# Optimization experiments

Hardware: AMD Instinct MI355X
Metric: run time of the kernel (lower is better)

The kernel has to match this reference:

```python
import jax, jax.numpy as jnp
import numpy as np

B = 8
A = 1614
TOPN = 6
IOU_THR = 0.25
PAD = 224
OUT = 224

def _make_anchors():
    # 6 anchor shapes on the 14x14 map, 6 on 7x7, 9 on 4x4 -> 1614 total,
    # ordered anchor-type-major then row-major spatial to match the [C,H,W] flatten
    # of the tidy conv outputs (as generate_default_anchor_maps does in NTS-Net).
    specs = [
        (14, 32.0, [(48, 48), (64, 48), (48, 64), (80, 80), (96, 64), (64, 96)]),
        (7, 64.0, [(96, 96), (128, 96), (96, 128), (160, 160), (192, 128), (128, 192)]),
        (4, 112.0, [(192, 192), (256, 192), (192, 256), (288, 288), (320, 256), (256, 320), (352, 352), (384, 320), (320, 384)]),
    ]
    blocks = []
    for fm, stride, sizes in specs:
        c = (np.arange(fm) + 0.5) * stride
        cy, cx = np.meshgrid(c, c, indexing='ij')
        for (h, w) in sizes:
            blocks.append(np.stack([cy - h / 2, cx - w / 2, cy + h / 2, cx + w / 2], -1).reshape(-1, 4))
    a = (np.concatenate(blocks, 0) + PAD).astype(np.int64)  # mimic (edge_anchors+224).astype(int)
    return a.astype(np.float32)  # [1614,4] (y0,x0,y1,x1) in padded-image coords

def _conv(x, w, b, stride, pad):
    y = jax.lax.conv_general_dilated(x, w, (stride, stride), [(pad, pad), (pad, pad)],
                                     dimension_numbers=('NCHW', 'OIHW', 'NCHW'))
    return y + b[None, :, None, None]

def _rpn_scores(rpn, wd1, bd1, wd2, bd2, wd3, bd3, wt1, bt1, wt2, bt2, wt3, bt3):
    b = rpn.shape[0]
    d1 = jax.nn.relu(_conv(rpn, wd1, bd1, 1, 1))   # [B,128,14,14]
    d2 = jax.nn.relu(_conv(d1, wd2, bd2, 2, 1))    # [B,128,7,7]
    d3 = jax.nn.relu(_conv(d2, wd3, bd3, 2, 1))    # [B,128,4,4]
    t1 = _conv(d1, wt1, bt1, 1, 0).reshape(b, -1)  # [B,1176]
    t2 = _conv(d2, wt2, bt2, 1, 0).reshape(b, -1)  # [B,294]
    t3 = _conv(d3, wt3, bt3, 1, 0).reshape(b, -1)  # [B,144]
    return jnp.concatenate([t1, t2, t3], axis=1)   # [B,1614]

def _nms_keep(boxes, scores):
    # Greedy NMS over all A anchors; returns keep mask in ORIGINAL anchor order.
    order = jnp.argsort(-scores)
    b = boxes[order]
    y0, x0, y1, x1 = b[:, 0], b[:, 1], b[:, 2], b[:, 3]
    area = (y1 - y0) * (x1 - x0)
    ih = jnp.clip(jnp.minimum(y1[:, None], y1[None, :]) - jnp.maximum(y0[:, None], y0[None, :]), 0)
    iw = jnp.clip(jnp.minimum(x1[:, None], x1[None, :]) - jnp.maximum(x0[:, None], x0[None, :]), 0)
    inter = ih * iw
    iou = inter / (area[:, None] + area[None, :] - inter)
    idx = jnp.arange(A)
    def body(i, supp):
        row = (iou[i] > IOU_THR) & (idx > i)
        return jnp.where(supp[i], supp, supp | row)
    supp = jax.lax.fori_loop(0, A, body, jnp.zeros((A,), bool))
    return jnp.zeros((A,), bool).at[order].set(~supp)

def _crop_resize(img, box):
    # img [3,Hp,Wp]; box int32 (x0,y0,x1,y1).
    # Equivalent to F.interpolate(img[:, y0:y1, x0:x1], (224,224), 'bilinear', align_corners=True)
    x0, y0, x1, y1 = box[0], box[1], box[2], box[3]
    t = jnp.arange(OUT, dtype=jnp.float32) / (OUT - 1)
    sy = y0.astype(jnp.float32) + t * (y1 - 1 - y0).astype(jnp.float32)
    sx = x0.astype(jnp.float32) + t * (x1 - 1 - x0).astype(jnp.float32)
    y0i = jnp.floor(sy).astype(jnp.int32); x0i = jnp.floor(sx).astype(jnp.int32)
    y1i = jnp.minimum(y0i + 1, y1 - 1);    x1i = jnp.minimum(x0i + 1, x1 - 1)
    wy = (sy - y0i.astype(jnp.float32))[None, :, None]
    wx = (sx - x0i.astype(jnp.float32))[None, None, :]
    g = lambda yi, xi: img[:, yi][:, :, xi]  # gather rows then cols -> [3,224,224]
    top = (1 - wx) * g(y0i, x0i) + wx * g(y0i, x1i)
    bot = (1 - wx) * g(y1i, x0i) + wx * g(y1i, x1i)
    return (1 - wy) * top + wy * bot

def setup_inputs():
    key = jax.random.key(0)
    ks = jax.random.split(key, 16)
    n = jax.random.normal
    return {
        'x': n(ks[0], (B, 3, 448, 448), jnp.float32),
        'rpn_feature': n(ks[1], (B, 2048, 14, 14), jnp.float32),
        'anchors': jnp.asarray(_make_anchors()),
        'wd1': 0.02 * n(ks[2], (128, 2048, 3, 3), jnp.float32), 'bd1': 0.01 * n(ks[3], (128,), jnp.float32),
        'wd2': 0.05 * n(ks[4], (128, 128, 3, 3), jnp.float32),  'bd2': 0.01 * n(ks[5], (128,), jnp.float32),
        'wd3': 0.05 * n(ks[6], (128, 128, 3, 3), jnp.float32),  'bd3': 0.01 * n(ks[7], (128,), jnp.float32),
        'wt1': 0.1 * n(ks[8], (6, 128, 1, 1), jnp.float32),     'bt1': 0.01 * n(ks[9], (6,), jnp.float32),
        'wt2': 0.1 * n(ks[10], (6, 128, 1, 1), jnp.float32),    'bt2': 0.01 * n(ks[11], (6,), jnp.float32),
        'wt3': 0.1 * n(ks[12], (9, 128, 1, 1), jnp.float32),    'bt3': 0.01 * n(ks[13], (9,), jnp.float32),
    }

def reference(x, rpn_feature, anchors, wd1, bd1, wd2, bd2, wd3, bd3, wt1, bt1, wt2, bt2, wt3, bt3):
    scores = _rpn_scores(rpn_feature, wd1, bd1, wd2, bd2, wd3, bd3, wt1, bt1, wt2, bt2, wt3, bt3)
    keep = jax.vmap(lambda s: _nms_keep(anchors, s))(scores)           # [B,A] bool
    masked = jnp.where(keep, scores, -jnp.inf)
    top_prob, top_idx = jax.lax.top_k(masked, TOPN)                    # [B,6]
    tb = anchors[top_idx]                                              # [B,6,4] (y0,x0,y1,x1)
    coords = jnp.stack([tb[..., 1], tb[..., 0], tb[..., 3], tb[..., 2]], -1)  # (x0,y0,x1,y1)
    x_pad = jnp.pad(x, ((0, 0), (0, 0), (PAD, PAD), (PAD, PAD)))       # [B,3,896,896]
    bint = coords.astype(jnp.int32)
    part_imgs = jax.vmap(lambda img, bs: jax.vmap(lambda bb: _crop_resize(img, bb))(bs))(x_pad, bint)  # [B,6,3,224,224]
    return part_imgs, coords, top_prob, top_idx
```

## Files before the change

kernel.cpp:

```cpp
#include <hip/hip_runtime.h>
#include <hip/hip_bf16.h>
#include <math.h>
#include <stdint.h>


#define OFF_COORDS 7225344
#define OFF_PROB   7225536
#define OFF_IDX    7225584
#define NA 1614
#define K1TOT 18432

typedef __attribute__((ext_vector_type(8)))  short  short8;
typedef __attribute__((ext_vector_type(16))) float  floatx16;

__device__ inline void split_bf16(float v, unsigned short& h, unsigned short& l)
{
    __hip_bfloat16 hb = __float2bfloat16(v);
    float hv = __bfloat162float(hb);
    __hip_bfloat16 lb = __float2bfloat16(v - hv);
    h = *reinterpret_cast<unsigned short*>(&hb);
    l = *reinterpret_cast<unsigned short*>(&lb);
}

__global__ __launch_bounds__(256) void k_prep_a(const float* __restrict__ rpn,
                                                __hip_bfloat16* __restrict__ ah,
                                                __hip_bfloat16* __restrict__ al)
{
    __shared__ float tile[64][65];
    const int cib  = blockIdx.x * 64;
    const int posb = blockIdx.y * 64;
    const int b    = blockIdx.z;
    const int t    = threadIdx.x;
#pragma unroll
    for (int it = 0; it < 16; ++it) {
        int idx  = it * 256 + t;
        int cil  = idx >> 6;
        int posl = idx & 63;
        int pos  = posb + posl;
        int py = pos >> 4, px = pos & 15;
        int y = py - 1, x = px - 1;
        float v = 0.0f;
        if ((unsigned)y < 14u && (unsigned)x < 14u)
            v = rpn[((size_t)(b * 2048 + cib + cil) * 14 + y) * 14 + x];
        tile[cil][posl] = v;
    }
    __syncthreads();
#pragma unroll
    for (int it = 0; it < 16; ++it) {
        int idx  = it * 256 + t;
        int posl = idx >> 6;
        int cil  = idx & 63;
        float v = tile[cil][posl];
        unsigned short h, l;
        split_bf16(v, h, l);
        size_t o = (size_t)(b * 256 + posb + posl) * 2048 + cib + cil;
        ((unsigned short*)ah)[o] = h;
        ((unsigned short*)al)[o] = l;
    }
}

__global__ __launch_bounds__(256) void k_prep_b(const float* __restrict__ w,
                                                __hip_bfloat16* __restrict__ bh,
                                                __hip_bfloat16* __restrict__ bl)
{
    __shared__ float tile[9][260];
    const int ci0 = blockIdx.x * 256;
    const int co  = blockIdx.y;
    const int t   = threadIdx.x;
    const float* wc = w + (size_t)co * K1TOT + (size_t)ci0 * 9;
#pragma unroll
    for (int it = 0; it < 9; ++it) {
        int i = it * 256 + t;
        float v = wc[i];
        tile[i % 9][i / 9] = v;
    }
    __syncthreads();
#pragma unroll
    for (int tap = 0; tap < 9; ++tap) {
        float v = tile[tap][t];
        unsigned short h, l;
        split_bf16(v, h, l);
        size_t o = (size_t)co * K1TOT + (size_t)tap * 2048 + ci0 + t;
        ((unsigned short*)bh)[o] = h;
        ((unsigned short*)bl)[o] = l;
    }
}

__global__ __launch_bounds__(128) void k_prep_w23(const float* __restrict__ w2,
                                                  const float* __restrict__ w3,
                                                  __hip_bfloat16* __restrict__ b2h,
                                                  __hip_bfloat16* __restrict__ b2l,
                                                  __hip_bfloat16* __restrict__ b3h,
                                                  __hip_bfloat16* __restrict__ b3l)
{
    const int tap = blockIdx.x;
    const int co  = blockIdx.y;
    const int z   = blockIdx.z;
    const int ci  = threadIdx.x;
    const float* w = z ? w3 : w2;
    __hip_bfloat16* bh = z ? b3h : b2h;
    __hip_bfloat16* bl = z ? b3l : b2l;
    float v = w[((size_t)co * 128 + ci) * 9 + tap];
    unsigned short h, l;
    split_bf16(v, h, l);
    size_t o = (size_t)co * 1152 + tap * 128 + ci;
    ((unsigned short*)bh)[o] = h;
    ((unsigned short*)bl)[o] = l;
}

template<int POSN, int OW, int STR, int CIN, int MTOT, int GX>
__global__ __launch_bounds__(256) void k_conv_mfma(const short* __restrict__ ah,
                                                   const short* __restrict__ al,
                                                   const short* __restrict__ bh,
                                                   const short* __restrict__ bl,
                                                   float* __restrict__ partial,
                                                   int chunk)
{
    constexpr int KTOT = CIN * 9;
    __shared__ short AsH[128][40];
    __shared__ short AsL[128][40];
    __shared__ short BsH[128][40];
    __shared__ short BsL[128][40];

    const int t     = threadIdx.x;
    const int lane  = t & 63;
    const int w     = t >> 6;
    const int wm    = (w & 1) * 64;
    const int wn    = (w >> 1) * 64;
    const int lm    = lane & 31;
    const int half  = lane >> 5;

    const int nb = gridDim.x;
    const int id = blockIdx.x;
    int mb, kc;
    if ((nb % (8 * GX)) == 0) {
        int xcd = id & 7;
        int j   = id >> 3;
        int jq  = j / GX;
        mb = j - jq * GX;
        kc = xcd + 8 * jq;
    } else {
        kc = id / GX;
        mb = id - kc * GX;
    }
    const int mbase = mb * 128;
    const int k0    = kc * chunk;
    const int k1    = (k0 + chunk < KTOT) ? (k0 + chunk) : KTOT;

    int arow[2], apos[2]; bool aval[2];
    const int akc = (t & 3) * 8;
#pragma unroll
    for (int i = 0; i < 2; ++i) {
        int row = ((i * 256 + t) >> 2);
        int m   = mbase + row;
        arow[i] = row;
        aval[i] = (m < MTOT);
        int mm = aval[i] ? m : 0;
        int b  = mm / POSN;
        int p  = mm - b * POSN;
        int y  = p / OW;
        int x  = p - y * OW;
        apos[i] = b * 256 + y * STR * 16 + x * STR;
    }

    floatx16 acc[2][2];
#pragma unroll
    for (int mf = 0; mf < 2; ++mf)
#pragma unroll
        for (int nf = 0; nf < 2; ++nf)
#pragma unroll
            for (int r = 0; r < 16; ++r) acc[mf][nf][r] = 0.0f;

    const short8 zero8 = {0, 0, 0, 0, 0, 0, 0, 0};
    short8 rAh[2], rAl[2], rBh[2], rBl[2];

    auto stage_load = [&](int ks) {
        const int tap = ks / CIN;
        const int ci0 = ks - tap * CIN;
        const int dy  = tap / 3, dx = tap - dy * 3;
#pragma unroll
        for (int i = 0; i < 2; ++i) {
            if (aval[i]) {
                size_t g = (size_t)(apos[i] + dy * 16 + dx) * CIN + ci0 + akc;
                rAh[i] = *(const short8*)(ah + g);
                rAl[i] = *(const short8*)(al + g);
            } else { rAh[i] = zero8; rAl[i] = zero8; }
        }
#pragma unroll
        for (int i = 0; i < 2; ++i) {
            int n = ((i * 256 + t) >> 2);
            size_t g = (size_t)n * KTOT + ks + akc;
            rBh[i] = *(const short8*)(bh + g);
            rBl[i] = *(const short8*)(bl + g);
        }
    };

    if (k0 < k1) stage_load(k0);

    for (int ks = k0; ks < k1; ks += 32) {
#pragma unroll
        for (int i = 0; i < 2; ++i) {
            *(short8*)&AsH[arow[i]][akc] = rAh[i];
            *(short8*)&AsL[arow[i]][akc] = rAl[i];
        }
#pragma unroll
        for (int i = 0; i < 2; ++i) {
            int n = ((i * 256 + t) >> 2);
            *(short8*)&BsH[n][akc] = rBh[i];
            *(short8*)&BsL[n][akc] = rBl[i];
        }
        __syncthreads();
        if (ks + 32 < k1) stage_load(ks + 32);
#pragma unroll
        for (int kst = 0; kst < 2; ++kst) {
            const int koff = kst * 16 + half * 8;
            short8 a_h[2], a_l[2], b_h[2], b_l[2];
#pragma unroll
            for (int mf = 0; mf < 2; ++mf) {
                a_h[mf] = *(const short8*)&AsH[wm + mf * 32 + lm][koff];
                a_l[mf] = *(const short8*)&AsL[wm + mf * 32 + lm][koff];
            }
#pragma unroll
            for (int nf = 0; nf < 2; ++nf) {
                b_h[nf] = *(const short8*)&BsH[wn + nf * 32 + lm][koff];
                b_l[nf] = *(const short8*)&BsL[wn + nf * 32 + lm][koff];
            }
#pragma unroll
            for (int mf = 0; mf < 2; ++mf)
#pragma unroll
                for (int nf = 0; nf < 2; ++nf) {
                    acc[mf][nf] = __builtin_amdgcn_mfma_f32_32x32x16_bf16(
                        a_h[mf], b_h[nf], acc[mf][nf], 0, 0, 0);
                    acc[mf][nf] = __builtin_amdgcn_mfma_f32_32x32x16_bf16(
                        a_h[mf], b_l[nf], acc[mf][nf], 0, 0, 0);
                    acc[mf][nf] = __builtin_amdgcn_mfma_f32_32x32x16_bf16(
                        a_l[mf], b_h[nf], acc[mf][nf], 0, 0, 0);
                }
        }
        __syncthreads();
    }

    float* P = partial + (size_t)kc * MTOT * 128;
#pragma unroll
    for (int mf = 0; mf < 2; ++mf)
#pragma unroll
        for (int nf = 0; nf < 2; ++nf)
#pragma unroll
            for (int r = 0; r < 16; ++r) {
                int row = (r & 3) + 8 * (r >> 2) + 4 * half;
                int m = mbase + wm + mf * 32 + row;
                int n = wn + nf * 32 + lm;
                if (m < MTOT) P[(size_t)m * 128 + n] = acc[mf][nf][r];
            }
}

template<int POSN, int OWV>
__global__ __launch_bounds__(256) void k_reduce_pad(const float* __restrict__ partial,
                                                    const float* __restrict__ bias,
                                                    float* __restrict__ dn,
                                                    __hip_bfloat16* __restrict__ ph,
                                                    __hip_bfloat16* __restrict__ pl,
                                                    int S)
{
    constexpr int MTOT = 8 * POSN;
    int idx = blockIdx.x * 256 + threadIdx.x;
    int b   = idx >> 13;
    int pos = (idx >> 5) & 255;
    int c4  = idx & 31;
    int y = (pos >> 4) - 1;
    int x = (pos & 15) - 1;
    if ((unsigned)y < (unsigned)OWV && (unsigned)x < (unsigned)OWV) {
        int m = b * POSN + y * OWV + x;
        float4 s = ((const float4*)bias)[c4];
        for (int k = 0; k < S; ++k) {
            float4 p = ((const float4*)(partial + (size_t)k * MTOT * 128 + (size_t)m * 128))[c4];
            s.x += p.x; s.y += p.y; s.z += p.z; s.w += p.w;
        }
        s.x = fmaxf(s.x, 0.0f); s.y = fmaxf(s.y, 0.0f);
        s.z = fmaxf(s.z, 0.0f); s.w = fmaxf(s.w, 0.0f);
        ((float4*)dn)[(size_t)m * 32 + c4] = s;
        ushort4 h, l;
        split_bf16(s.x, h.x, l.x);
        split_bf16(s.y, h.y, l.y);
        split_bf16(s.z, h.z, l.z);
        split_bf16(s.w, h.w, l.w);
        ((ushort4*)ph)[idx] = h;
        ((ushort4*)pl)[idx] = l;
    } else {
        ushort4 z = {0, 0, 0, 0};
        ((ushort4*)ph)[idx] = z;
        ((ushort4*)pl)[idx] = z;
    }
}

__global__ __launch_bounds__(256) void k_reduce3(const float* __restrict__ partial,
                                                 const float* __restrict__ bias,
                                                 float* __restrict__ dn, int S)
{
    int idx = blockIdx.x * 256 + threadIdx.x;
    int c4  = idx & 31;
    float4 s = ((const float4*)bias)[c4];
    for (int k = 0; k < S; ++k) {
        float4 p = ((const float4*)(partial + (size_t)k * 128 * 128))[idx];
        s.x += p.x; s.y += p.y; s.z += p.z; s.w += p.w;
    }
    s.x = fmaxf(s.x, 0.0f); s.y = fmaxf(s.y, 0.0f);
    s.z = fmaxf(s.z, 0.0f); s.w = fmaxf(s.w, 0.0f);
    ((float4*)dn)[idx] = s;
}

__global__ __launch_bounds__(256) void k_heads(const float* __restrict__ d1n,
                                               const float* __restrict__ d2n,
                                               const float* __restrict__ d3n,
                                               const float* __restrict__ w1, const float* __restrict__ b1,
                                               const float* __restrict__ w2, const float* __restrict__ b2,
                                               const float* __restrict__ w3, const float* __restrict__ b3,
                                               float* __restrict__ scores)
{
    int idx = blockIdx.x * 256 + threadIdx.x;
    if (idx >= 8 * NA) return;
    int b = idx / NA;
    int e = idx - b * NA;
    const float* d; const float* w; float bias;
    if (e < 1176) {
        int c = e / 196, p = e - c * 196;
        d = d1n + (size_t)(b * 196 + p) * 128; w = w1 + c * 128; bias = b1[c];
    } else if (e < 1470) {
        int e2 = e - 1176; int c = e2 / 49, p = e2 - c * 49;
        d = d2n + (size_t)(b * 49 + p) * 128; w = w2 + c * 128; bias = b2[c];
    } else {
        int e2 = e - 1470; int c = e2 / 16, p = e2 - c * 16;
        d = d3n + (size_t)(b * 16 + p) * 128; w = w3 + c * 128; bias = b3[c];
    }
    float s = bias;
#pragma unroll
    for (int i = 0; i < 32; ++i) {
        float4 dv = ((const float4*)d)[i];
        float4 wv = ((const float4*)w)[i];
        s = fmaf(dv.x, wv.x, s);
        s = fmaf(dv.y, wv.y, s);
        s = fmaf(dv.z, wv.z, s);
        s = fmaf(dv.w, wv.w, s);
    }
    scores[idx] = s;
}

__global__ __launch_bounds__(256) void k_nms_topk(const float* __restrict__ scores,
                                                  const float* __restrict__ anchors,
                                                  float* __restrict__ out,
                                                  int* __restrict__ boxes)
{
    __shared__ float ms[NA];
    __shared__ float ay0[NA], ax0[NA], ay1[NA], ax1[NA];
    __shared__ unsigned char picked[NA];
    __shared__ float rv[4]; __shared__ int ri[4];
    __shared__ float win[5];
    int b = blockIdx.x;
    int t = threadIdx.x;
    for (int i = t; i < NA; i += 256) {
        ms[i] = scores[b * NA + i];
        float4 an = ((const float4*)anchors)[i];
        ay0[i] = an.x; ax0[i] = an.y; ay1[i] = an.z; ax1[i] = an.w;
        picked[i] = 0;
    }
    __syncthreads();
    for (int r = 0; r < 6; ++r) {
        float bv = -INFINITY; int bi = NA;
        for (int i = t; i < NA; i += 256) {
            if (!picked[i]) {
                float v = ms[i];
                if (v > bv || (v == bv && i < bi)) { bv = v; bi = i; }
            }
        }
#pragma unroll
        for (int off = 32; off > 0; off >>= 1) {
            float v2 = __shfl_down(bv, off);
            int   i2 = __shfl_down(bi, off);
            if (v2 > bv || (v2 == bv && i2 < bi)) { bv = v2; bi = i2; }
        }
        if ((t & 63) == 0) { rv[t >> 6] = bv; ri[t >> 6] = bi; }
        __syncthreads();
        if (t == 0) {
            bv = rv[0]; bi = ri[0];
            for (int wv = 1; wv < 4; ++wv)
                if (rv[wv] > bv || (rv[wv] == bv && ri[wv] < bi)) { bv = rv[wv]; bi = ri[wv]; }
            picked[bi] = 1;
            win[0] = ay0[bi]; win[1] = ax0[bi]; win[2] = ay1[bi]; win[3] = ax1[bi]; win[4] = bv;
            int o = b * 6 + r;
            out[OFF_COORDS + o * 4 + 0] = ax0[bi];
            out[OFF_COORDS + o * 4 + 1] = ay0[bi];
            out[OFF_COORDS + o * 4 + 2] = ax1[bi];
            out[OFF_COORDS + o * 4 + 3] = ay1[bi];
            out[OFF_PROB + o] = bv;
            out[OFF_IDX  + o] = (float)bi;
            boxes[o * 4 + 0] = (int)ax0[bi];
            boxes[o * 4 + 1] = (int)ay0[bi];
            boxes[o * 4 + 2] = (int)ax1[bi];
            boxes[o * 4 + 3] = (int)ay1[bi];
        }
        __syncthreads();
        float by0 = win[0], bx0 = win[1], by1 = win[2], bx1 = win[3];
        float barea = (by1 - by0) * (bx1 - bx0);
        for (int i = t; i < NA; i += 256) {
            if (picked[i]) continue;
            float ih = fmaxf(fminf(by1, ay1[i]) - fmaxf(by0, ay0[i]), 0.0f);
            float iw = fmaxf(fminf(bx1, ax1[i]) - fmaxf(bx0, ax0[i]), 0.0f);
            float inter = ih * iw;
            float area  = (ay1[i] - ay0[i]) * (ax1[i] - ax0[i]);
            float iou = inter / (barea + area - inter);
            if (iou > 0.25f) ms[i] = -INFINITY;
        }
        __syncthreads();
    }
}

__global__ __launch_bounds__(256) void k_crop(const float* __restrict__ x,
                                              const int* __restrict__ boxes,
                                              float* __restrict__ out)
{
    int bid = blockIdx.x;
    int i = threadIdx.x;
    if (i >= 224) return;
    int j   = bid % 224;
    int rem = bid / 224;
    int c   = rem % 3;
    int br  = rem / 3;
    int b   = br / 6;
    int4 bx = ((const int4*)boxes)[br];
    float tj = (float)j / 223.0f;
    float sy = (float)bx.y + tj * (float)(bx.w - 1 - bx.y);
    int y0i = (int)floorf(sy);
    int y1i = min(y0i + 1, bx.w - 1);
    float wy = sy - (float)y0i;
    float ti = (float)i / 223.0f;
    float sx = (float)bx.x + ti * (float)(bx.z - 1 - bx.x);
    int x0i = (int)floorf(sx);
    int x1i = min(x0i + 1, bx.z - 1);
    float wx = sx - (float)x0i;
    const float* img = x + ((size_t)b * 3 + c) * 448 * 448;
    auto g = [&](int yy, int xx) -> float {
        yy -= 224; xx -= 224;
        if ((unsigned)yy >= 448u || (unsigned)xx >= 448u) return 0.0f;
        return img[(size_t)yy * 448 + xx];
    };
    float g00 = g(y0i, x0i), g01 = g(y0i, x1i);
    float g10 = g(y1i, x0i), g11 = g(y1i, x1i);
    float top = (1.0f - wx) * g00 + wx * g01;
    float bot = (1.0f - wx) * g10 + wx * g11;
    out[(size_t)bid * 224 + i] = (1.0f - wy) * top + wy * bot;
}

extern "C" void kernel_launch(void* const* d_in, const int* in_sizes, int n_in,
                              void* d_out, int out_size, void* d_ws, size_t ws_size,
                              hipStream_t stream)
{
    (void)in_sizes; (void)n_in; (void)out_size;
    const float* x    = (const float*)d_in[0];
    const float* rpn  = (const float*)d_in[1];
    const float* anch = (const float*)d_in[2];
    const float* wd1  = (const float*)d_in[3];
    const float* bd1  = (const float*)d_in[4];
    const float* wd2  = (const float*)d_in[5];
    const float* bd2  = (const float*)d_in[6];
    const float* wd3  = (const float*)d_in[7];
    const float* bd3  = (const float*)d_in[8];
    const float* hw1  = (const float*)d_in[9];
    const float* hb1  = (const float*)d_in[10];
    const float* hw2  = (const float*)d_in[11];
    const float* hb2  = (const float*)d_in[12];
    const float* hw3  = (const float*)d_in[13];
    const float* hb3  = (const float*)d_in[14];
    float* out = (float*)d_out;

    char* ws = (char*)d_ws;
    size_t off = 0;
    auto alloc = [&](size_t bytes) -> void* {
        void* p = ws + off;
        off = (off + bytes + 255) & ~(size_t)255;
        return p;
    };
    __hip_bfloat16* ahb  = (__hip_bfloat16*)alloc((size_t)8 * 256 * 2048 * 2);
    __hip_bfloat16* alb  = (__hip_bfloat16*)alloc((size_t)8 * 256 * 2048 * 2);
    __hip_bfloat16* b1h  = (__hip_bfloat16*)alloc((size_t)128 * K1TOT * 2);
    __hip_bfloat16* b1l  = (__hip_bfloat16*)alloc((size_t)128 * K1TOT * 2);
    __hip_bfloat16* b2h  = (__hip_bfloat16*)alloc((size_t)128 * 1152 * 2);
    __hip_bfloat16* b2l  = (__hip_bfloat16*)alloc((size_t)128 * 1152 * 2);
    __hip_bfloat16* b3h  = (__hip_bfloat16*)alloc((size_t)128 * 1152 * 2);
    __hip_bfloat16* b3l  = (__hip_bfloat16*)alloc((size_t)128 * 1152 * 2);
    __hip_bfloat16* d1ph = (__hip_bfloat16*)alloc((size_t)8 * 256 * 128 * 2);
    __hip_bfloat16* d1pl = (__hip_bfloat16*)alloc((size_t)8 * 256 * 128 * 2);
    __hip_bfloat16* d2ph = (__hip_bfloat16*)alloc((size_t)8 * 256 * 128 * 2);
    __hip_bfloat16* d2pl = (__hip_bfloat16*)alloc((size_t)8 * 256 * 128 * 2);
    float* d1n  = (float*)alloc((size_t)8 * 196 * 128 * 4);
    float* d2n  = (float*)alloc((size_t)8 * 49 * 128 * 4);
    float* d3n  = (float*)alloc((size_t)8 * 16 * 128 * 4);
    float* sc   = (float*)alloc((size_t)8 * NA * 4);
    int*  boxes = (int*)alloc((size_t)8 * 6 * 4 * 4);
    size_t avail = (ws_size > off) ? (ws_size - off) : 0;
    float* P = (float*)(ws + off);

    long long s1 = (long long)(avail / ((size_t)1568 * 128 * 4));
    if (s1 > 48) s1 = 48;
    if (s1 < 1)  s1 = 1;
    int S1 = (int)s1;
    int chunk1 = ((K1TOT + S1 * 32 - 1) / (S1 * 32)) * 32;

    k_prep_b<<<dim3(8, 128), 256, 0, stream>>>(wd1, b1h, b1l);
    k_prep_w23<<<dim3(9, 128, 2), 128, 0, stream>>>(wd2, wd3, b2h, b2l, b3h, b3l);
    k_prep_a<<<dim3(32, 4, 8), 256, 0, stream>>>(rpn, ahb, alb);

    k_conv_mfma<196, 14, 1, 2048, 1568, 13><<<dim3(13 * S1), 256, 0, stream>>>(
        (const short*)ahb, (const short*)alb, (const short*)b1h, (const short*)b1l, P, chunk1);
    k_reduce_pad<196, 14><<<dim3(256), 256, 0, stream>>>(P, bd1, d1n, d1ph, d1pl, S1);

    k_conv_mfma<49, 7, 2, 128, 392, 4><<<dim3(36), 256, 0, stream>>>(
        (const short*)d1ph, (const short*)d1pl, (const short*)b2h, (const short*)b2l, P, 128);
    k_reduce_pad<49, 7><<<dim3(256), 256, 0, stream>>>(P, bd2, d2n, d2ph, d2pl, 9);

    k_conv_mfma<16, 4, 2, 128, 128, 1><<<dim3(9), 256, 0, stream>>>(
        (const short*)d2ph, (const short*)d2pl, (const short*)b3h, (const short*)b3l, P, 128);
    k_reduce3<<<dim3(16), 256, 0, stream>>>(P, bd3, d3n, 9);

    k_heads<<<dim3((8 * NA + 255) / 256), 256, 0, stream>>>(d1n, d2n, d3n,
        hw1, hb1, hw2, hb2, hw3, hb3, sc);
    k_nms_topk<<<dim3(8), 256, 0, stream>>>(sc, anch, out, boxes);
    k_crop<<<dim3(8 * 6 * 3 * 224), 256, 0, stream>>>(x, boxes, out);
}
```

Before: 256.1 us.

## Fuse prep kernels, fold split-K reduction into conv, merge heads with NMS

Three prep kernels and the zeroing of the padded buffers are merged into one launch. The split-K reduction moves into the conv kernels through an atomic counter: the last block per M tile sums the partials and applies bias and ReLU. The conv kernels switch to a single swizzled LDS buffer with a wider K step and lose the register prefetch. Heads are fused into the 512-thread NMS kernel, and crop now uses every thread of each block. This removes several launches and intermediate round trips, at the cost of serialized tail reductions and a conv main loop that no longer overlaps loads with compute.

```diff
diff --git a/kernel.cpp b/kernel.cpp
--- a/kernel.cpp
+++ b/kernel.cpp
@@ -22,145 +22,154 @@
     l = *reinterpret_cast<unsigned short*>(&lb);
 }
 
-__global__ __launch_bounds__(256) void k_prep_a(const float* __restrict__ rpn,
-                                                __hip_bfloat16* __restrict__ ah,
-                                                __hip_bfloat16* __restrict__ al)
+__global__ __launch_bounds__(256) void k_prep(const float* __restrict__ rpn,
+                                              const float* __restrict__ w1,
+                                              const float* __restrict__ w2,
+                                              const float* __restrict__ w3,
+                                              unsigned short* __restrict__ ah,
+                                              unsigned short* __restrict__ al,
+                                              unsigned short* __restrict__ b1h,
+                                              unsigned short* __restrict__ b1l,
+                                              unsigned short* __restrict__ b2h,
+                                              unsigned short* __restrict__ b2l,
+                                              unsigned short* __restrict__ b3h,
+                                              unsigned short* __restrict__ b3l,
+                                              short* __restrict__ z0,
+                                              short* __restrict__ z1,
+                                              short* __restrict__ z2,
+                                              short* __restrict__ z3,
+                                              int* __restrict__ cnt)
 {
-    __shared__ float tile[64][65];
-    const int cib  = blockIdx.x * 64;
-    const int posb = blockIdx.y * 64;
-    const int b    = blockIdx.z;
-    const int t    = threadIdx.x;
-#pragma unroll
-    for (int it = 0; it < 16; ++it) {
-        int idx  = it * 256 + t;
-        int cil  = idx >> 6;
-        int posl = idx & 63;
-        int pos  = posb + posl;
-        int py = pos >> 4, px = pos & 15;
-        int y = py - 1, x = px - 1;
-        float v = 0.0f;
-        if ((unsigned)y < 14u && (unsigned)x < 14u)
-            v = rpn[((size_t)(b * 2048 + cib + cil) * 14 + y) * 14 + x];
-        tile[cil][posl] = v;
-    }
-    __syncthreads();
-#pragma unroll
-    for (int it = 0; it < 16; ++it) {
-        int idx  = it * 256 + t;
-        int posl = idx >> 6;
-        int cil  = idx & 63;
-        float v = tile[cil][posl];
+    __shared__ float tileA[64][65];
+    __shared__ float tileB[9][260];
+    const int bid = blockIdx.x;
+    const int t   = threadIdx.x;
+
+    if (bid < 1024) {
+        const int cib  = (bid & 31) * 64;
+        const int posb = ((bid >> 5) & 3) * 64;
+        const int b    = bid >> 7;
+#pragma unroll
+        for (int it = 0; it < 16; ++it) {
+            int idx  = it * 256 + t;
+            int cil  = idx >> 6;
+            int posl = idx & 63;
+            int pos  = posb + posl;
+            int py = pos >> 4, px = pos & 15;
+            int y = py - 1, x = px - 1;
+            float v = 0.0f;
+            if ((unsigned)y < 14u && (unsigned)x < 14u)
+                v = rpn[((size_t)(b * 2048 + cib + cil) * 14 + y) * 14 + x];
+            tileA[cil][posl] = v;
+        }
+        __syncthreads();
+#pragma unroll
+        for (int it = 0; it < 16; ++it) {
+            int idx  = it * 256 + t;
+            int posl = idx >> 6;
+            int cil  = idx & 63;
+            float v = tileA[cil][posl];
+            unsigned short h, l;
+            split_bf16(v, h, l);
+            size_t o = (size_t)(b * 256 + posb + posl) * 2048 + cib + cil;
+            ah[o] = h; al[o] = l;
+        }
+    } else if (bid < 2048) {
+        const int lb  = bid - 1024;
+        const int ci0 = (lb & 7) * 256;
+        const int co  = lb >> 3;
+        const float* wc = w1 + (size_t)co * K1TOT + (size_t)ci0 * 9;
+#pragma unroll
+        for (int it = 0; it < 9; ++it) {
+            int i = it * 256 + t;
+            float v = wc[i];
+            tileB[i % 9][i / 9] = v;
+        }
+        __syncthreads();
+#pragma unroll
+        for (int tap = 0; tap < 9; ++tap) {
+            float v = tileB[tap][t];
+            unsigned short h, l;
+            split_bf16(v, h, l);
+            size_t o = (size_t)co * K1TOT + (size_t)tap * 2048 + ci0 + t;
+            b1h[o] = h; b1l[o] = l;
+        }
+    } else if (bid < 3200) {
+        const int lb  = bid - 2048;
+        const int tap = lb % 9;
+        const int co  = lb / 9;
+        const int z   = t >> 7;
+        const int ci  = t & 127;
+        const float* w = z ? w3 : w2;
+        unsigned short* bh = z ? b3h : b2h;
+        unsigned short* bl = z ? b3l : b2l;
+        float v = w[((size_t)co * 128 + ci) * 9 + tap];
         unsigned short h, l;
         split_bf16(v, h, l);
-        size_t o = (size_t)(b * 256 + posb + posl) * 2048 + cib + cil;
-        ((unsigned short*)ah)[o] = h;
-        ((unsigned short*)al)[o] = l;
+        size_t o = (size_t)co * 1152 + tap * 128 + ci;
+        bh[o] = h; bl[o] = l;
+    } else if (bid < 3712) {
+        const int lb  = bid - 3200;
+        short* z = (lb < 128) ? z0 : (lb < 256) ? z1 : (lb < 384) ? z2 : z3;
+        const short8 zero8 = {0,0,0,0,0,0,0,0};
+        ((short8*)z)[(size_t)(lb & 127) * 256 + t] = zero8;
+    } else {
+        if (t < 32) cnt[t] = 0;
     }
 }
 
-__global__ __launch_bounds__(256) void k_prep_b(const float* __restrict__ w,
-                                                __hip_bfloat16* __restrict__ bh,
-                                                __hip_bfloat16* __restrict__ bl)
+template<int POSN, int OW, int STR, int CIN, int MTOT, int KSTEP, int S, int PADOUT>
+__global__ __launch_bounds__(256) void k_conv_red(const short* __restrict__ ah,
+                                                  const short* __restrict__ al,
+                                                  const short* __restrict__ bh,
+                                                  const short* __restrict__ bl,
+                                                  float* __restrict__ partial,
+                                                  int* __restrict__ cnt,
+                                                  const float* __restrict__ bias,
+                                                  float* __restrict__ dn,
+                                                  __hip_bfloat16* __restrict__ ph,
+                                                  __hip_bfloat16* __restrict__ pl)
 {
-    __shared__ float tile[9][260];
-    const int ci0 = blockIdx.x * 256;
-    const int co  = blockIdx.y;
-    const int t   = threadIdx.x;
-    const float* wc = w + (size_t)co * K1TOT + (size_t)ci0 * 9;
-#pragma unroll
-    for (int it = 0; it < 9; ++it) {
-        int i = it * 256 + t;
-        float v = wc[i];
-        tile[i % 9][i / 9] = v;
-    }
-    __syncthreads();
-#pragma unroll
-    for (int tap = 0; tap < 9; ++tap) {
-        float v = tile[tap][t];
-        unsigned short h, l;
-        split_bf16(v, h, l);
-        size_t o = (size_t)co * K1TOT + (size_t)tap * 2048 + ci0 + t;
-        ((unsigned short*)bh)[o] = h;
-        ((unsigned short*)bl)[o] = l;
-    }
-}
-
-__global__ __launch_bounds__(128) void k_prep_w23(const float* __restrict__ w2,
-                                                  const float* __restrict__ w3,
-                                                  __hip_bfloat16* __restrict__ b2h,
-                                                  __hip_bfloat16* __restrict__ b2l,
-                                                  __hip_bfloat16* __restrict__ b3h,
-                                                  __hip_bfloat16* __restrict__ b3l)
-{
-    const int tap = blockIdx.x;
-    const int co  = blockIdx.y;
-    const int z   = blockIdx.z;
-    const int ci  = threadIdx.x;
-    const float* w = z ? w3 : w2;
-    __hip_bfloat16* bh = z ? b3h : b2h;
-    __hip_bfloat16* bl = z ? b3l : b2l;
-    float v = w[((size_t)co * 128 + ci) * 9 + tap];
-    unsigned short h, l;
-    split_bf16(v, h, l);
-    size_t o = (size_t)co * 1152 + tap * 128 + ci;
-    ((unsigned short*)bh)[o] = h;
-    ((unsigned short*)bl)[o] = l;
-}
-
-template<int POSN, int OW, int STR, int CIN, int MTOT, int GX>
-__global__ __launch_bounds__(256) void k_conv_mfma(const short* __restrict__ ah,
-                                                   const short* __restrict__ al,
-                                                   const short* __restrict__ bh,
-                                                   const short* __restrict__ bl,
-                                                   float* __restrict__ partial,
-                                                   int chunk)
-{
-    constexpr int KTOT = CIN * 9;
-    __shared__ short AsH[128][40];
-    __shared__ short AsL[128][40];
-    __shared__ short BsH[128][40];
-    __shared__ short BsL[128][40];
-
-    const int t     = threadIdx.x;
-    const int lane  = t & 63;
-    const int w     = t >> 6;
-    const int wm    = (w & 1) * 64;
-    const int wn    = (w >> 1) * 64;
-    const int lm    = lane & 31;
-    const int half  = lane >> 5;
-
-    const int nb = gridDim.x;
-    const int id = blockIdx.x;
-    int mb, kc;
-    if ((nb % (8 * GX)) == 0) {
-        int xcd = id & 7;
-        int j   = id >> 3;
-        int jq  = j / GX;
-        mb = j - jq * GX;
-        kc = xcd + 8 * jq;
-    } else {
-        kc = id / GX;
-        mb = id - kc * GX;
-    }
+    constexpr int KTOT   = CIN * 9;
+    constexpr int CHUNK  = KTOT / S;
+    constexpr int NST    = CHUNK / KSTEP;
+    constexpr int NCH    = KSTEP / 8;
+    constexpr int TPR    = NCH;
+    constexpr int RPP    = 256 / TPR;
+    constexpr int PASSES = 128 / RPP;
+
+    __shared__ short Sm[4][128][KSTEP];
+
+    const int t    = threadIdx.x;
+    const int lane = t & 63;
+    const int w    = t >> 6;
+    const int wm   = (w & 1) * 64;
+    const int wn   = (w >> 1) * 64;
+    const int lm   = lane & 31;
+    const int half = lane >> 5;
+    const int mb   = blockIdx.x;
+    const int kc   = blockIdx.y;
     const int mbase = mb * 128;
-    const int k0    = kc * chunk;
-    const int k1    = (k0 + chunk < KTOT) ? (k0 + chunk) : KTOT;
-
-    int arow[2], apos[2]; bool aval[2];
-    const int akc = (t & 3) * 8;
-#pragma unroll
-    for (int i = 0; i < 2; ++i) {
-        int row = ((i * 256 + t) >> 2);
+    const int k0    = kc * CHUNK;
+
+    auto swz = [](int row, int c) -> int {
+        return (KSTEP == 64) ? (c ^ (row & 7)) : (c ^ ((row >> 1) & 3));
+    };
+
+    const int lr = t / TPR;
+    const int ck = t % TPR;
+    int apos[PASSES]; bool aval[PASSES];
+#pragma unroll
+    for (int p = 0; p < PASSES; ++p) {
+        int row = p * RPP + lr;
         int m   = mbase + row;
-        arow[i] = row;
-        aval[i] = (m < MTOT);
-        int mm = aval[i] ? m : 0;
+        aval[p] = (m < MTOT);
+        int mm = aval[p] ? m : 0;
         int b  = mm / POSN;
-        int p  = mm - b * POSN;
-        int y  = p / OW;
-        int x  = p - y * OW;
-        apos[i] = b * 256 + y * STR * 16 + x * STR;
+        int pp = mm - b * POSN;
+        int y  = pp / OW;
+        int x  = pp - y * OW;
+        apos[p] = b * 256 + y * STR * 16 + x * STR;
     }
 
     floatx16 acc[2][2];
@@ -172,58 +181,52 @@
             for (int r = 0; r < 16; ++r) acc[mf][nf][r] = 0.0f;
 
     const short8 zero8 = {0, 0, 0, 0, 0, 0, 0, 0};
-    short8 rAh[2], rAl[2], rBh[2], rBl[2];
-
-    auto stage_load = [&](int ks) {
+
+    for (int st = 0; st < NST; ++st) {
+        const int ks  = k0 + st * KSTEP;
         const int tap = ks / CIN;
         const int ci0 = ks - tap * CIN;
         const int dy  = tap / 3, dx = tap - dy * 3;
-#pragma unroll
-        for (int i = 0; i < 2; ++i) {
-            if (aval[i]) {
-                size_t g = (size_t)(apos[i] + dy * 16 + dx) * CIN + ci0 + akc;
-                rAh[i] = *(const short8*)(ah + g);
-                rAl[i] = *(const short8*)(al + g);
-            } else { rAh[i] = zero8; rAl[i] = zero8; }
-        }
-#pragma unroll
-        for (int i = 0; i < 2; ++i) {
-            int n = ((i * 256 + t) >> 2);
-            size_t g = (size_t)n * KTOT + ks + akc;
-            rBh[i] = *(const short8*)(bh + g);
-            rBl[i] = *(const short8*)(bl + g);
-        }
-    };
-
-    if (k0 < k1) stage_load(k0);
-
-    for (int ks = k0; ks < k1; ks += 32) {
-#pragma unroll
-        for (int i = 0; i < 2; ++i) {
-            *(short8*)&AsH[arow[i]][akc] = rAh[i];
-            *(short8*)&AsL[arow[i]][akc] = rAl[i];
-        }
-#pragma unroll
-        for (int i = 0; i < 2; ++i) {
-            int n = ((i * 256 + t) >> 2);
-            *(short8*)&BsH[n][akc] = rBh[i];
-            *(short8*)&BsL[n][akc] = rBl[i];
-        }
-        __syncthreads();
-        if (ks + 32 < k1) stage_load(ks + 32);
-#pragma unroll
-        for (int kst = 0; kst < 2; ++kst) {
-            const int koff = kst * 16 + half * 8;
+        short8 vah[PASSES], val_[PASSES], vbh[PASSES], vbl[PASSES];
+#pragma unroll
+        for (int p = 0; p < PASSES; ++p) {
+            int row = p * RPP + lr;
+            if (aval[p]) {
+                size_t g = (size_t)(apos[p] + dy * 16 + dx) * CIN + ci0 + ck * 8;
+                vah[p] = *(const short8*)(ah + g);
+                val_[p] = *(const short8*)(al + g);
+            } else { vah[p] = zero8; val_[p] = zero8; }
+            size_t gb = (size_t)row * KTOT + ks + ck * 8;
+            vbh[p] = *(const short8*)(bh + gb);
+            vbl[p] = *(const short8*)(bl + gb);
+        }
+#pragma unroll
+        for (int p = 0; p < PASSES; ++p) {
+            int row = p * RPP + lr;
+            int sc  = swz(row, ck) * 8;
+            *(short8*)&Sm[0][row][sc] = vah[p];
+            *(short8*)&Sm[1][row][sc] = val_[p];
+            *(short8*)&Sm[2][row][sc] = vbh[p];
+            *(short8*)&Sm[3][row][sc] = vbl[p];
+        }
+        __syncthreads();
+#pragma unroll
+        for (int kst = 0; kst < KSTEP / 16; ++kst) {
+            const int c = kst * 2 + half;
             short8 a_h[2], a_l[2], b_h[2], b_l[2];
 #pragma unroll
             for (int mf = 0; mf < 2; ++mf) {
-                a_h[mf] = *(const short8*)&AsH[wm + mf * 32 + lm][koff];
-                a_l[mf] = *(const short8*)&AsL[wm + mf * 32 + lm][koff];
+                int r = wm + mf * 32 + lm;
+                int sc = swz(r, c) * 8;
+                a_h[mf] = *(const short8*)&Sm[0][r][sc];
+                a_l[mf] = *(const short8*)&Sm[1][r][sc];
             }
 #pragma unroll
             for (int nf = 0; nf < 2; ++nf) {
-                b_h[nf] = *(const short8*)&BsH[wn + nf * 32 + lm][koff];
-                b_l[nf] = *(const short8*)&BsL[wn + nf * 32 + lm][koff];
+                int r = wn + nf * 32 + lm;
+                int sc = swz(r, c) * 8;
+                b_h[nf] = *(const short8*)&Sm[2][r][sc];
+                b_l[nf] = *(const short8*)&Sm[3][r][sc];
             }
 #pragma unroll
             for (int mf = 0; mf < 2; ++mf)
@@ -252,121 +255,105 @@
                 int n = wn + nf * 32 + lm;
                 if (m < MTOT) P[(size_t)m * 128 + n] = acc[mf][nf][r];
             }
-}
-
-template<int POSN, int OWV>
-__global__ __launch_bounds__(256) void k_reduce_pad(const float* __restrict__ partial,
-                                                    const float* __restrict__ bias,
-                                                    float* __restrict__ dn,
-                                                    __hip_bfloat16* __restrict__ ph,
-                                                    __hip_bfloat16* __restrict__ pl,
-                                                    int S)
-{
-    constexpr int MTOT = 8 * POSN;
-    int idx = blockIdx.x * 256 + threadIdx.x;
-    int b   = idx >> 13;
-    int pos = (idx >> 5) & 255;
-    int c4  = idx & 31;
-    int y = (pos >> 4) - 1;
-    int x = (pos & 15) - 1;
-    if ((unsigned)y < (unsigned)OWV && (unsigned)x < (unsigned)OWV) {
-        int m = b * POSN + y * OWV + x;
+
+    __threadfence();
+    int* flagp = (int*)&Sm[0][0][0];
+    if (t == 0) *flagp = (atomicAdd(cnt + mb, 1) == S - 1) ? 1 : 0;
+    __syncthreads();
+    if (!*flagp) return;
+    __threadfence();
+#pragma unroll 1
+    for (int slot = t; slot < 128 * 32; slot += 256) {
+        int row = slot >> 5;
+        int c4  = slot & 31;
+        int m   = mbase + row;
+        if (m >= MTOT) continue;
         float4 s = ((const float4*)bias)[c4];
         for (int k = 0; k < S; ++k) {
-            float4 p = ((const float4*)(partial + (size_t)k * MTOT * 128 + (size_t)m * 128))[c4];
-            s.x += p.x; s.y += p.y; s.z += p.z; s.w += p.w;
+            const float4 pv = *(const float4*)(partial +
+                ((size_t)k * MTOT + m) * 128 + c4 * 4);
+            s.x += pv.x; s.y += pv.y; s.z += pv.z; s.w += pv.w;
         }
         s.x = fmaxf(s.x, 0.0f); s.y = fmaxf(s.y, 0.0f);
         s.z = fmaxf(s.z, 0.0f); s.w = fmaxf(s.w, 0.0f);
         ((float4*)dn)[(size_t)m * 32 + c4] = s;
-        ushort4 h, l;
-        split_bf16(s.x, h.x, l.x);
-        split_bf16(s.y, h.y, l.y);
-        split_bf16(s.z, h.z, l.z);
-        split_bf16(s.w, h.w, l.w);
-        ((ushort4*)ph)[idx] = h;
-        ((ushort4*)pl)[idx] = l;
-    } else {
-        ushort4 z = {0, 0, 0, 0};
-        ((ushort4*)ph)[idx] = z;
-        ((ushort4*)pl)[idx] = z;
+        if (PADOUT) {
+            int b = m / POSN;
+            int p = m - b * POSN;
+            int y = p / OW;
+            int x = p - y * OW;
+            size_t pidx = (size_t)(b * 256 + (y + 1) * 16 + (x + 1)) * 32 + c4;
+            ushort4 h, l;
+            split_bf16(s.x, h.x, l.x);
+            split_bf16(s.y, h.y, l.y);
+            split_bf16(s.z, h.z, l.z);
+            split_bf16(s.w, h.w, l.w);
+            ((ushort4*)ph)[pidx] = h;
+            ((ushort4*)pl)[pidx] = l;
+        }
     }
 }
 
-__global__ __launch_bounds__(256) void k_reduce3(const float* __restrict__ partial,
-                                                 const float* __restrict__ bias,
-                                                 float* __restrict__ dn, int S)
-{
-    int idx = blockIdx.x * 256 + threadIdx.x;
-    int c4  = idx & 31;
-    float4 s = ((const float4*)bias)[c4];
-    for (int k = 0; k < S; ++k) {
-        float4 p = ((const float4*)(partial + (size_t)k * 128 * 128))[idx];
-        s.x += p.x; s.y += p.y; s.z += p.z; s.w += p.w;
-    }
-    s.x = fmaxf(s.x, 0.0f); s.y = fmaxf(s.y, 0.0f);
-    s.z = fmaxf(s.z, 0.0f); s.w = fmaxf(s.w, 0.0f);
-    ((float4*)dn)[idx] = s;
-}
-
-__global__ __launch_bounds__(256) void k_heads(const float* __restrict__ d1n,
-                                               const float* __restrict__ d2n,
-                                               const float* __restrict__ d3n,
-                                               const float* __restrict__ w1, const float* __restrict__ b1,
-                                               const float* __restrict__ w2, const float* __restrict__ b2,
-                                               const float* __restrict__ w3, const float* __restrict__ b3,
-                                               float* __restrict__ scores)
-{
-    int idx = blockIdx.x * 256 + threadIdx.x;
-    if (idx >= 8 * NA) return;
-    int b = idx / NA;
-    int e = idx - b * NA;
-    const float* d; const float* w; float bias;
-    if (e < 1176) {
-        int c = e / 196, p = e - c * 196;
-        d = d1n + (size_t)(b * 196 + p) * 128; w = w1 + c * 128; bias = b1[c];
-    } else if (e < 1470) {
-        int e2 = e - 1176; int c = e2 / 49, p = e2 - c * 49;
-        d = d2n + (size_t)(b * 49 + p) * 128; w = w2 + c * 128; bias = b2[c];
-    } else {
-        int e2 = e - 1470; int c = e2 / 16, p = e2 - c * 16;
-        d = d3n + (size_t)(b * 16 + p) * 128; w = w3 + c * 128; bias = b3[c];
-    }
-    float s = bias;
-#pragma unroll
-    for (int i = 0; i < 32; ++i) {
-        float4 dv = ((const float4*)d)[i];
-        float4 wv = ((const float4*)w)[i];
-        s = fmaf(dv.x, wv.x, s);
-        s = fmaf(dv.y, wv.y, s);
-        s = fmaf(dv.z, wv.z, s);
-        s = fmaf(dv.w, wv.w, s);
-    }
-    scores[idx] = s;
-}
-
-__global__ __launch_bounds__(256) void k_nms_topk(const float* __restrict__ scores,
-                                                  const float* __restrict__ anchors,
-                                                  float* __restrict__ out,
-                                                  int* __restrict__ boxes)
+__global__ __launch_bounds__(512) void k_headnms(const float* __restrict__ d1n,
+                                                 const float* __restrict__ d2n,
+                                                 const float* __restrict__ d3n,
+                                                 const float* __restrict__ w1, const float* __restrict__ b1,
+                                                 const float* __restrict__ w2, const float* __restrict__ b2,
+                                                 const float* __restrict__ w3, const float* __restrict__ b3,
+                                                 const float* __restrict__ anchors,
+                                                 float* __restrict__ out,
+                                                 int* __restrict__ boxes)
 {
     __shared__ float ms[NA];
     __shared__ float ay0[NA], ax0[NA], ay1[NA], ax1[NA];
     __shared__ unsigned char picked[NA];
-    __shared__ float rv[4]; __shared__ int ri[4];
+    __shared__ float wsm[21 * 128];
+    __shared__ float bsm[21];
+    __shared__ float rv[8]; __shared__ int ri[8];
     __shared__ float win[5];
-    int b = blockIdx.x;
-    int t = threadIdx.x;
-    for (int i = t; i < NA; i += 256) {
-        ms[i] = scores[b * NA + i];
+    const int b = blockIdx.x;
+    const int t = threadIdx.x;
+
+    for (int i = t; i < 21 * 128; i += 512)
+        wsm[i] = (i < 768) ? w1[i] : (i < 1536) ? w2[i - 768] : w3[i - 1536];
+    if (t < 21) bsm[t] = (t < 6) ? b1[t] : (t < 12) ? b2[t - 6] : b3[t - 12];
+    for (int i = t; i < NA; i += 512) {
         float4 an = ((const float4*)anchors)[i];
         ay0[i] = an.x; ax0[i] = an.y; ay1[i] = an.z; ax1[i] = an.w;
         picked[i] = 0;
     }
     __syncthreads();
+
+    for (int e = t; e < NA; e += 512) {
+        const float* d; int wrow;
+        if (e < 1176) {
+            int c = e / 196, p = e - c * 196;
+            d = d1n + (size_t)(b * 196 + p) * 128; wrow = c;
+        } else if (e < 1470) {
+            int e2 = e - 1176; int c = e2 / 49, p = e2 - c * 49;
+            d = d2n + (size_t)(b * 49 + p) * 128; wrow = 6 + c;
+        } else {
+            int e2 = e - 1470; int c = e2 / 16, p = e2 - c * 16;
+            d = d3n + (size_t)(b * 16 + p) * 128; wrow = 12 + c;
+        }
+        float s = bsm[wrow];
+        const float4* wv4 = (const float4*)&wsm[wrow * 128];
+#pragma unroll
+        for (int i = 0; i < 32; ++i) {
+            float4 dv = ((const float4*)d)[i];
+            float4 wv = wv4[i];
+            s = fmaf(dv.x, wv.x, s);
+            s = fmaf(dv.y, wv.y, s);
+            s = fmaf(dv.z, wv.z, s);
+            s = fmaf(dv.w, wv.w, s);
+        }
+        ms[e] = s;
+    }
+    __syncthreads();
+
     for (int r = 0; r < 6; ++r) {
         float bv = -INFINITY; int bi = NA;
-        for (int i = t; i < NA; i += 256) {
+        for (int i = t; i < NA; i += 512) {
             if (!picked[i]) {
                 float v = ms[i];
                 if (v > bv || (v == bv && i < bi)) { bv = v; bi = i; }
@@ -382,7 +369,7 @@
         __syncthreads();
         if (t == 0) {
             bv = rv[0]; bi = ri[0];
-            for (int wv = 1; wv < 4; ++wv)
+            for (int wv = 1; wv < 8; ++wv)
                 if (rv[wv] > bv || (rv[wv] == bv && ri[wv] < bi)) { bv = rv[wv]; bi = ri[wv]; }
             picked[bi] = 1;
             win[0] = ay0[bi]; win[1] = ax0[bi]; win[2] = ay1[bi]; win[3] = ax1[bi]; win[4] = bv;
@@ -401,7 +388,7 @@
         __syncthreads();
         float by0 = win[0], bx0 = win[1], by1 = win[2], bx1 = win[3];
         float barea = (by1 - by0) * (bx1 - bx0);
-        for (int i = t; i < NA; i += 256) {
+        for (int i = t; i < NA; i += 512) {
             if (picked[i]) continue;
             float ih = fmaxf(fminf(by1, ay1[i]) - fmaxf(by0, ay0[i]), 0.0f);
             float iw = fmaxf(fminf(bx1, ax1[i]) - fmaxf(bx0, ax0[i]), 0.0f);
@@ -418,11 +405,10 @@
                                               const int* __restrict__ boxes,
                                               float* __restrict__ out)
 {
-    int bid = blockIdx.x;
-    int i = threadIdx.x;
-    if (i >= 224) return;
-    int j   = bid % 224;
-    int rem = bid / 224;
+    int idx = blockIdx.x * 256 + threadIdx.x;
+    int i   = idx % 224;
+    int j   = (idx / 224) % 224;
+    int rem = idx / 50176;
     int c   = rem % 3;
     int br  = rem / 3;
     int b   = br / 6;
@@ -447,14 +433,14 @@
     float g10 = g(y1i, x0i), g11 = g(y1i, x1i);
     float top = (1.0f - wx) * g00 + wx * g01;
     float bot = (1.0f - wx) * g10 + wx * g11;
-    out[(size_t)bid * 224 + i] = (1.0f - wy) * top + wy * bot;
+    out[idx] = (1.0f - wy) * top + wy * bot;
 }
 
 extern "C" void kernel_launch(void* const* d_in, const int* in_sizes, int n_in,
                               void* d_out, int out_size, void* d_ws, size_t ws_size,
                               hipStream_t stream)
 {
-    (void)in_sizes; (void)n_in; (void)out_size;
+    (void)in_sizes; (void)n_in; (void)out_size; (void)ws_size;
     const float* x    = (const float*)d_in[0];
     const float* rpn  = (const float*)d_in[1];
     const float* anch = (const float*)d_in[2];
@@ -479,14 +465,14 @@
         off = (off + bytes + 255) & ~(size_t)255;
         return p;
     };
-    __hip_bfloat16* ahb  = (__hip_bfloat16*)alloc((size_t)8 * 256 * 2048 * 2);
-    __hip_bfloat16* alb  = (__hip_bfloat16*)alloc((size_t)8 * 256 * 2048 * 2);
-    __hip_bfloat16* b1h  = (__hip_bfloat16*)alloc((size_t)128 * K1TOT * 2);
-    __hip_bfloat16* b1l  = (__hip_bfloat16*)alloc((size_t)128 * K1TOT * 2);
-    __hip_bfloat16* b2h  = (__hip_bfloat16*)alloc((size_t)128 * 1152 * 2);
-    __hip_bfloat16* b2l  = (__hip_bfloat16*)alloc((size_t)128 * 1152 * 2);
-    __hip_bfloat16* b3h  = (__hip_bfloat16*)alloc((size_t)128 * 1152 * 2);
-    __hip_bfloat16* b3l  = (__hip_bfloat16*)alloc((size_t)128 * 1152 * 2);
+    unsigned short* ahb = (unsigned short*)alloc((size_t)8 * 256 * 2048 * 2);
+    unsigned short* alb = (unsigned short*)alloc((size_t)8 * 256 * 2048 * 2);
+    unsigned short* b1h = (unsigned short*)alloc((size_t)128 * K1TOT * 2);
+    unsigned short* b1l = (unsigned short*)alloc((size_t)128 * K1TOT * 2);
+    unsigned short* b2h = (unsigned short*)alloc((size_t)128 * 1152 * 2);
+    unsigned short* b2l = (unsigned short*)alloc((size_t)128 * 1152 * 2);
+    unsigned short* b3h = (unsigned short*)alloc((size_t)128 * 1152 * 2);
+    unsigned short* b3l = (unsigned short*)alloc((size_t)128 * 1152 * 2);
     __hip_bfloat16* d1ph = (__hip_bfloat16*)alloc((size_t)8 * 256 * 128 * 2);
     __hip_bfloat16* d1pl = (__hip_bfloat16*)alloc((size_t)8 * 256 * 128 * 2);
     __hip_bfloat16* d2ph = (__hip_bfloat16*)alloc((size_t)8 * 256 * 128 * 2);
@@ -494,35 +480,28 @@
     float* d1n  = (float*)alloc((size_t)8 * 196 * 128 * 4);
     float* d2n  = (float*)alloc((size_t)8 * 49 * 128 * 4);
     float* d3n  = (float*)alloc((size_t)8 * 16 * 128 * 4);
-    float* sc   = (float*)alloc((size_t)8 * NA * 4);
+    int*   cnt  = (int*)alloc(32 * 4);
     int*  boxes = (int*)alloc((size_t)8 * 6 * 4 * 4);
-    size_t avail = (ws_size > off) ? (ws_size - off) : 0;
-    float* P = (float*)(ws + off);
-
-    long long s1 = (long long)(avail / ((size_t)1568 * 128 * 4));
-    if (s1 > 48) s1 = 48;
-    if (s1 < 1)  s1 = 1;
-    int S1 = (int)s1;
-    int chunk1 = ((K1TOT + S1 * 32 - 1) / (S1 * 32)) * 32;
-
-    k_prep_b<<<dim3(8, 128), 256, 0, stream>>>(wd1, b1h, b1l);
-    k_prep_w23<<<dim3(9, 128, 2), 128, 0, stream>>>(wd2, wd3, b2h, b2l, b3h, b3l);
-    k_prep_a<<<dim3(32, 4, 8), 256, 0, stream>>>(rpn, ahb, alb);
-
-    k_conv_mfma<196, 14, 1, 2048, 1568, 13><<<dim3(13 * S1), 256, 0, stream>>>(
-        (const short*)ahb, (const short*)alb, (const short*)b1h, (const short*)b1l, P, chunk1);
-    k_reduce_pad<196, 14><<<dim3(256), 256, 0, stream>>>(P, bd1, d1n, d1ph, d1pl, S1);
-
-    k_conv_mfma<49, 7, 2, 128, 392, 4><<<dim3(36), 256, 0, stream>>>(
-        (const short*)d1ph, (const short*)d1pl, (const short*)b2h, (const short*)b2l, P, 128);
-    k_reduce_pad<49, 7><<<dim3(256), 256, 0, stream>>>(P, bd2, d2n, d2ph, d2pl, 9);
-
-    k_conv_mfma<16, 4, 2, 128, 128, 1><<<dim3(9), 256, 0, stream>>>(
-        (const short*)d2ph, (const short*)d2pl, (const short*)b3h, (const short*)b3l, P, 128);
-    k_reduce3<<<dim3(16), 256, 0, stream>>>(P, bd3, d3n, 9);
-
-    k_heads<<<dim3((8 * NA + 255) / 256), 256, 0, stream>>>(d1n, d2n, d3n,
-        hw1, hb1, hw2, hb2, hw3, hb3, sc);
-    k_nms_topk<<<dim3(8), 256, 0, stream>>>(sc, anch, out, boxes);
-    k_crop<<<dim3(8 * 6 * 3 * 224), 256, 0, stream>>>(x, boxes, out);
+    float* P    = (float*)alloc((size_t)48 * 1568 * 128 * 4);
+
+    k_prep<<<dim3(3713), 256, 0, stream>>>(rpn, wd1, wd2, wd3,
+        ahb, alb, b1h, b1l, b2h, b2l, b3h, b3l,
+        (short*)d1ph, (short*)d1pl, (short*)d2ph, (short*)d2pl, cnt);
+
+    k_conv_red<196, 14, 1, 2048, 1568, 64, 48, 1><<<dim3(13, 48), 256, 0, stream>>>(
+        (const short*)ahb, (const short*)alb, (const short*)b1h, (const short*)b1l,
+        P, cnt, bd1, d1n, d1ph, d1pl);
+
+    k_conv_red<49, 7, 2, 128, 392, 32, 36, 1><<<dim3(4, 36), 256, 0, stream>>>(
+        (const short*)d1ph, (const short*)d1pl, (const short*)b2h, (const short*)b2l,
+        P, cnt + 16, bd2, d2n, d2ph, d2pl);
+
+    k_conv_red<16, 4, 2, 128, 128, 32, 36, 0><<<dim3(1, 36), 256, 0, stream>>>(
+        (const short*)d2ph, (const short*)d2pl, (const short*)b3h, (const short*)b3l,
+        P, cnt + 24, bd3, d3n, nullptr, nullptr);
+
+    k_headnms<<<dim3(8), 512, 0, stream>>>(d1n, d2n, d3n,
+        hw1, hb1, hw2, hb2, hw3, hb3, anch, out, boxes);
+
+    k_crop<<<dim3(28224), 256, 0, stream>>>(x, boxes, out);
 }
```

Measured after the change: 433.2 us. +69.2%, slower.
